# Optimization experiments

Hardware: AMD Instinct MI355X
Metric: run time of the kernel (lower is better)

Reference implementation:

```python
import jax, jax.numpy as jnp
import numpy as np
import itertools

DIM_X, DIM_Y = 3, 3
MAX_DIGIT = DIM_X * DIM_Y          # 9
NUM_NODES = MAX_DIGIT ** 2         # 81
EMBED = 16
HID = 96
BATCH = 256
ITERS = 4


def determine_edges(dim_x, dim_y):
    md = dim_x * dim_y
    rows = []
    for r in range(md):
        for c in range(md):
            s = {(r, i) for i in range(md)} | {(i, c) for i in range(md)}
            xm, ym = r // dim_x * dim_x, c // dim_y * dim_y
            s |= set(itertools.product(range(xm, xm + dim_x), range(ym, ym + dim_y)))
            s -= {(r, c)}
            rows.append(sorted(i * md + j for i, j in s))
    return np.asarray(rows, dtype=np.int32)  # [81, 20]


def mlp3(x, w0, b0, w1, b1, w2, b2):
    # MLP([a,b,c,d]): two ReLU hidden layers, linear output
    x = jax.nn.relu(x @ w0.T + b0)
    x = jax.nn.relu(x @ w1.T + b1)
    return x @ w2.T + b2


def setup_inputs() -> dict:
    key = jax.random.key(0)
    keys = iter(jax.random.split(key, 40))

    def lin(din, dout):
        kw, kb = jax.random.split(next(keys))
        lim = 1.0 / np.sqrt(din)
        w = jax.random.uniform(kw, (dout, din), jnp.float32, -lim, lim)
        b = jax.random.uniform(kb, (dout,), jnp.float32, -lim, lim)
        return w, b

    embed = jax.random.normal(next(keys), (MAX_DIGIT + 1, EMBED), jnp.float32)

    in_w0, in_b0 = lin(EMBED, HID); in_w1, in_b1 = lin(HID, HID); in_w2, in_b2 = lin(HID, HID)
    f_w0, f_b0 = lin(2 * HID, HID); f_w1, f_b1 = lin(HID, HID); f_w2, f_b2 = lin(HID, HID)
    g_w0, g_b0 = lin(2 * HID, HID); g_w1, g_b1 = lin(HID, HID); g_w2, g_b2 = lin(HID, HID)
    r_w0, r_b0 = lin(HID, HID); r_w1, r_b1 = lin(HID, HID); r_w2, r_b2 = lin(HID, MAX_DIGIT)

    lim = 1.0 / np.sqrt(HID)
    lstm_wih = jax.random.uniform(next(keys), (4 * HID, HID), jnp.float32, -lim, lim)
    lstm_whh = jax.random.uniform(next(keys), (4 * HID, HID), jnp.float32, -lim, lim)
    lstm_bih = jax.random.uniform(next(keys), (4 * HID,), jnp.float32, -lim, lim)
    lstm_bhh = jax.random.uniform(next(keys), (4 * HID,), jnp.float32, -lim, lim)

    grids = jax.random.randint(next(keys), (BATCH, NUM_NODES), 0, MAX_DIGIT + 1)
    c0 = jax.random.normal(next(keys), (BATCH * NUM_NODES, HID), jnp.float32)
    edges = jnp.asarray(determine_edges(DIM_X, DIM_Y))

    return dict(embed=embed,
                in_w0=in_w0, in_b0=in_b0, in_w1=in_w1, in_b1=in_b1, in_w2=in_w2, in_b2=in_b2,
                f_w0=f_w0, f_b0=f_b0, f_w1=f_w1, f_b1=f_b1, f_w2=f_w2, f_b2=f_b2,
                g_w0=g_w0, g_b0=g_b0, g_w1=g_w1, g_b1=g_b1, g_w2=g_w2, g_b2=g_b2,
                lstm_wih=lstm_wih, lstm_whh=lstm_whh, lstm_bih=lstm_bih, lstm_bhh=lstm_bhh,
                r_w0=r_w0, r_b0=r_b0, r_w1=r_w1, r_b1=r_b1, r_w2=r_w2, r_b2=r_b2,
                c0=c0, grids=grids, edges=edges, iters=ITERS)


def reference(embed,
              in_w0, in_b0, in_w1, in_b1, in_w2, in_b2,
              f_w0, f_b0, f_w1, f_b1, f_w2, f_b2,
              g_w0, g_b0, g_w1, g_b1, g_w2, g_b2,
              lstm_wih, lstm_whh, lstm_bih, lstm_bhh,
              r_w0, r_b0, r_w1, r_b1, r_w2, r_b2,
              c0, grids, edges, iters):
    B, N = grids.shape
    K = edges.shape[1]
    emb = embed[grids]                                   # [B, N, EMBED]
    X = mlp3(emb, in_w0, in_b0, in_w1, in_b1, in_w2, in_b2)  # [B, N, HID]
    H = X
    h = X.reshape(B * N, HID)
    c = c0
    outputs = []
    for _ in range(iters):
        # gather neighbor states: [B, N, K, HID]
        Hn = H[:, edges]
        Hs = jnp.broadcast_to(H[:, :, None, :], Hn.shape)
        pair = jnp.concatenate([Hs, Hn], axis=-1)        # [B, N, K, 2*HID]
        M = mlp3(pair, f_w0, f_b0, f_w1, f_b1, f_w2, f_b2).sum(axis=2)  # [B, N, HID]
        gin = mlp3(jnp.concatenate([X, M], axis=-1),
                   g_w0, g_b0, g_w1, g_b1, g_w2, g_b2).reshape(B * N, HID)
        # single-step LSTM (torch gate order: i, f, g, o)
        gates = gin @ lstm_wih.T + lstm_bih + h @ lstm_whh.T + lstm_bhh
        gi, gf, gg, go = jnp.split(gates, 4, axis=-1)
        c = jax.nn.sigmoid(gf) * c + jax.nn.sigmoid(gi) * jnp.tanh(gg)
        h = jax.nn.sigmoid(go) * jnp.tanh(c)
        H = h.reshape(B, N, HID)
        outputs.append(mlp3(H, r_w0, r_b0, r_w1, r_b1, r_w2, r_b2))  # [B, N, MAX_DIGIT]
    return jnp.stack(outputs)  # [iters, B, N, MAX_DIGIT]
```

## Files before the change

kernel.cpp:

```cpp
#include <hip/hip_runtime.h>
#include <hip/hip_bf16.h>

typedef __hip_bfloat16 bf16;
typedef __attribute__((ext_vector_type(8))) short short8;
typedef __attribute__((ext_vector_type(8))) __bf16 bf16x8;
typedef __attribute__((ext_vector_type(4))) float f32x4;

#define BN 20736
#define NNODE 81
#define KNB 20

__device__ inline float bf2f(short s) {
  union { unsigned u; float f; } x; x.u = ((unsigned)(unsigned short)s) << 16; return x.f;
}
__device__ inline short f2bf(float f) {
  __hip_bfloat16 h = __float2bfloat16(f);
  return *reinterpret_cast<short*>(&h);
}

__device__ inline void zacc3(f32x4 acc[3]) {
  #pragma unroll
  for (int nt = 0; nt < 3; ++nt) acc[nt] = (f32x4){0.f, 0.f, 0.f, 0.f};
}
__device__ inline void load_w48(const bf16* __restrict__ W, int ldw, int n0, int lr, int lq,
                                bf16x8 wf[3][3]) {
  #pragma unroll
  for (int nt = 0; nt < 3; ++nt)
    #pragma unroll
    for (int ks = 0; ks < 3; ++ks)
      wf[nt][ks] = __builtin_bit_cast(bf16x8,
          *(const short8*)&W[(size_t)(n0 + nt * 16 + lr) * ldw + ks * 32 + lq * 8]);
}
__device__ inline void gemm48(const bf16x8 af[3], const bf16x8 wf[3][3], f32x4 acc[3]) {
  #pragma unroll
  for (int ks = 0; ks < 3; ++ks)
    #pragma unroll
    for (int nt = 0; nt < 3; ++nt)
      acc[nt] = __builtin_amdgcn_mfma_f32_16x16x32_bf16(af[ks], wf[nt][ks], acc[nt], 0, 0, 0);
}
__device__ inline void acc_store_cs(float* xw, const f32x4 acc[3], int lr, int lq, int n0) {
  #pragma unroll
  for (int nt = 0; nt < 3; ++nt)
    #pragma unroll
    for (int r = 0; r < 4; ++r)
      xw[(lq * 4 + r) * 100 + n0 + nt * 16 + lr] = acc[nt][r];
}
__device__ inline void xbuf_frag(const float* xw, int lr, int lq,
                                 const float* __restrict__ bias, float bscale,
                                 const bf16* __restrict__ residRow, int act,
                                 bf16x8 af[3]) {
  #pragma unroll
  for (int ks = 0; ks < 3; ++ks) {
    const int c0 = ks * 32 + lq * 8;
    float4 x0 = *(const float4*)&xw[lr * 100 + c0];
    float4 x1 = *(const float4*)&xw[lr * 100 + c0 + 4];
    float xv[8] = {x0.x, x0.y, x0.z, x0.w, x1.x, x1.y, x1.z, x1.w};
    if (bias) {
      float4 b0 = *(const float4*)&bias[c0];
      float4 b1 = *(const float4*)&bias[c0 + 4];
      float bv[8] = {b0.x, b0.y, b0.z, b0.w, b1.x, b1.y, b1.z, b1.w};
      #pragma unroll
      for (int j = 0; j < 8; ++j) xv[j] += bscale * bv[j];
    }
    if (residRow) {
      short8 r8 = *(const short8*)&residRow[c0];
      #pragma unroll
      for (int j = 0; j < 8; ++j) xv[j] += bf2f(r8[j]);
    }
    short8 o;
    #pragma unroll
    for (int j = 0; j < 8; ++j) {
      float v = xv[j];
      if (act) v = fmaxf(v, 0.f);
      o[j] = f2bf(v);
    }
    af[ks] = __builtin_bit_cast(bf16x8, o);
  }
}
__device__ inline void store_frag(bf16* dst, int lq, const bf16x8 af[3]) {
  #pragma unroll
  for (int ks = 0; ks < 3; ++ks)
    *(short8*)&dst[ks * 32 + lq * 8] = __builtin_bit_cast(short8, af[ks]);
}

__global__ __launch_bounds__(256) void prep_k(
    const float* in_w1, const float* in_w2, const float* f_w1, const float* f_w2,
    const float* g_w1, const float* g_w2, const float* r_w0, const float* r_w1,
    const float* r_w2, const float* wih, const float* whh, const float* g_w0,
    const float* f_w0, const float* in_w0, const float* f_b0,
    bf16* inw1b, bf16* inw2b, bf16* fw1b, bf16* fw2b,
    bf16* gw1b, bf16* gw2b, bf16* rw0b, bf16* rw1b,
    bf16* rw2b, bf16* wihb, bf16* whhb, bf16* gw0b,
    bf16* wfnb, bf16* w0pb, float* bias_fn)
{
  int idx = blockIdx.x * 256 + threadIdx.x;
  int y = blockIdx.y;
  const float* src = nullptr; bf16* dst = nullptr; int cnt = 0;
  switch (y) {
    case 0:  src = in_w1; dst = inw1b; cnt = 9216;  break;
    case 1:  src = in_w2; dst = inw2b; cnt = 9216;  break;
    case 2:  src = f_w1;  dst = fw1b;  cnt = 9216;  break;
    case 3:  src = f_w2;  dst = fw2b;  cnt = 9216;  break;
    case 4:  src = g_w1;  dst = gw1b;  cnt = 9216;  break;
    case 5:  src = g_w2;  dst = gw2b;  cnt = 9216;  break;
    case 6:  src = r_w0;  dst = rw0b;  cnt = 9216;  break;
    case 7:  src = r_w1;  dst = rw1b;  cnt = 9216;  break;
    case 8:  src = r_w2;  dst = rw2b;  cnt = 864;   break;
    case 9:  src = wih;   dst = wihb;  cnt = 36864; break;
    case 10: src = whh;   dst = whhb;  cnt = 36864; break;
    case 11: src = g_w0;  dst = gw0b;  cnt = 18432; break;
    case 12: {
      if (idx < 18432) {
        int n = idx / 96, k = idx - n * 96;
        float v = (n < 96) ? f_w0[n * 192 + k] : f_w0[(n - 96) * 192 + 96 + k];
        wfnb[idx] = __float2bfloat16(v);
      }
      return;
    }
    case 13: {
      if (idx < 3072) {
        int n = idx >> 5, k = idx & 31;
        w0pb[idx] = __float2bfloat16(k < 16 ? in_w0[n * 16 + k] : 0.f);
      }
      return;
    }
    default: {
      if (idx < 192) bias_fn[idx] = (idx < 96) ? f_b0[idx] : 0.f;
      return;
    }
  }
  if (idx < cnt) dst[idx] = __float2bfloat16(src[idx]);
}

__global__ __launch_bounds__(256) void embed_k(const float* __restrict__ embed,
                                               const int* __restrict__ grids,
                                               bf16* __restrict__ emb) {
  int idx = blockIdx.x * 256 + threadIdx.x;
  if (idx >= BN * 32) return;
  int r = idx >> 5, k = idx & 31;
  emb[idx] = __float2bfloat16(k < 16 ? embed[grids[r] * 16 + k] : 0.f);
}

__global__ __launch_bounds__(256) void fused_in_k(
    const bf16* __restrict__ emb, const bf16* __restrict__ w0pb, const float* __restrict__ in_b0,
    const bf16* __restrict__ inw1b, const float* __restrict__ in_b1,
    const bf16* __restrict__ inw2b, const float* __restrict__ in_b2,
    const bf16* __restrict__ gw0b, const float* __restrict__ g_b0,
    const bf16* __restrict__ wfnb, const float* __restrict__ bias_fn,
    bf16* __restrict__ X, bf16* __restrict__ Xg, bf16* __restrict__ P)
{
  __shared__ float xbuf[2][2][1600];
  const int t = threadIdx.x, w = t >> 6, lane = t & 63, lr = lane & 15, lq = lane >> 4;
  const int mh = w >> 1, ch = w & 1, n0 = ch * 48;
  const int m0 = blockIdx.x * 32 + mh * 16;
  float* x0 = xbuf[0][mh];
  float* x1 = xbuf[1][mh];
  bf16x8 wf[3][3]; f32x4 acc[3]; bf16x8 af[3];

  bf16x8 a0 = __builtin_bit_cast(bf16x8, *(const short8*)&emb[(size_t)(m0 + lr) * 32 + lq * 8]);
  #pragma unroll
  for (int nt = 0; nt < 3; ++nt)
    wf[nt][0] = __builtin_bit_cast(bf16x8,
        *(const short8*)&w0pb[(size_t)(n0 + nt * 16 + lr) * 32 + lq * 8]);
  zacc3(acc);
  #pragma unroll
  for (int nt = 0; nt < 3; ++nt)
    acc[nt] = __builtin_amdgcn_mfma_f32_16x16x32_bf16(a0, wf[nt][0], acc[nt], 0, 0, 0);
  acc_store_cs(x0, acc, lr, lq, n0);
  __syncthreads();
  xbuf_frag(x0, lr, lq, in_b0, 1.f, nullptr, 1, af);
  load_w48(inw1b, 96, n0, lr, lq, wf); zacc3(acc); gemm48(af, wf, acc);
  acc_store_cs(x1, acc, lr, lq, n0);
  __syncthreads();
  xbuf_frag(x1, lr, lq, in_b1, 1.f, nullptr, 1, af);
  load_w48(inw2b, 96, n0, lr, lq, wf); zacc3(acc); gemm48(af, wf, acc);
  acc_store_cs(x0, acc, lr, lq, n0);
  __syncthreads();
  bf16x8 xf[3];
  xbuf_frag(x0, lr, lq, in_b2, 1.f, nullptr, 0, xf);
  if (ch == 0) store_frag(&X[(size_t)(m0 + lr) * 96], lq, xf);
  load_w48(gw0b, 192, n0, lr, lq, wf); zacc3(acc); gemm48(xf, wf, acc);
  acc_store_cs(x1, acc, lr, lq, n0);
  __syncthreads();
  xbuf_frag(x1, lr, lq, g_b0, 1.f, nullptr, 0, af);
  if (ch == 0) store_frag(&Xg[(size_t)(m0 + lr) * 96], lq, af);
  #pragma unroll
  for (int ph = 0; ph < 2; ++ph) {
    float* xb = ph ? x1 : x0;
    load_w48(wfnb + (size_t)ph * 96 * 96, 96, n0, lr, lq, wf); zacc3(acc); gemm48(xf, wf, acc);
    acc_store_cs(xb, acc, lr, lq, n0);
    __syncthreads();
    xbuf_frag(xb, lr, lq, bias_fn + ph * 96, 1.f, nullptr, 0, af);
    if (ch == 0) store_frag(&P[(size_t)(m0 + lr) * 192 + ph * 96], lq, af);
  }
}

__global__ __launch_bounds__(256) void edge_k(
    const bf16* __restrict__ P, const bf16* __restrict__ w1bf,
    const float* __restrict__ b1, const int* __restrict__ edges,
    const bf16* __restrict__ fw2b, const float* __restrict__ f_b2,
    bf16* __restrict__ M)
{
  __shared__ short zs[160 * 104];
  __shared__ short sbuf[16 * 104];
  const int t = threadIdx.x;
  const int ng0 = blockIdx.x * 2;
  for (int i = t; i < 8 * 104; i += 256) sbuf[(8 + i / 104) * 104 + (i % 104)] = 0;
  for (int cc = t; cc < 160 * 12; cc += 256) {
    int zrow = cc / 12, c8 = cc - zrow * 12;
    int g = zrow >= 80 ? 1 : 0;
    int row = zrow - g * 80;
    int p = row / 20, j = row - p * 20;
    int gr = (ng0 + g) * 4 + p;
    int b = gr / NNODE, i = gr - b * NNODE;
    int e = edges[i * KNB + j];
    short8 a8 = *(const short8*)&P[(size_t)gr * 192 + c8 * 8];
    short8 n8 = *(const short8*)&P[((size_t)b * NNODE + e) * 192 + 96 + c8 * 8];
    short8 z;
    #pragma unroll
    for (int q = 0; q < 8; ++q)
      z[q] = f2bf(fmaxf(bf2f(a8[q]) + bf2f(n8[q]), 0.f));
    *(short8*)&zs[zrow * 104 + c8 * 8] = z;
  }
  __syncthreads();

  const int w = t >> 6, lane = t & 63, lr = lane & 15, lq = lane >> 4;
  const int g = w >> 1, ch = w & 1, n0 = ch * 48, zb = g * 80;

  bf16x8 wf[3][3];
  #pragma unroll
  for (int nt = 0; nt < 3; ++nt)
    #pragma unroll
    for (int ks = 0; ks < 3; ++ks)
      wf[nt][ks] = __builtin_bit_cast(bf16x8,
          *(const short8*)&w1bf[(size_t)(n0 + nt * 16 + lr) * 96 + ks * 32 + lq * 8]);

  f32x4 acc[5][3];
  #pragma unroll
  for (int mt = 0; mt < 5; ++mt)
    #pragma unroll
    for (int nt = 0; nt < 3; ++nt) acc[mt][nt] = (f32x4){0.f, 0.f, 0.f, 0.f};

  #pragma unroll
  for (int ks = 0; ks < 3; ++ks) {
    const int koff = ks * 32 + lq * 8;
    #pragma unroll
    for (int mt = 0; mt < 5; ++mt) {
      bf16x8 af = __builtin_bit_cast(bf16x8, *(const short8*)&zs[(zb + mt * 16 + lr) * 104 + koff]);
      #pragma unroll
      for (int nt = 0; nt < 3; ++nt)
        acc[mt][nt] = __builtin_amdgcn_mfma_f32_16x16x32_bf16(af, wf[nt][ks], acc[mt][nt], 0, 0, 0);
    }
  }

  float bv[3];
  #pragma unroll
  for (int nt = 0; nt < 3; ++nt) bv[nt] = b1[n0 + nt * 16 + lr];
  float nodeacc[4][3];
  #pragma unroll
  for (int pp = 0; pp < 4; ++pp)
    #pragma unroll
    for (int nt = 0; nt < 3; ++nt) nodeacc[pp][nt] = 0.f;
  #pragma unroll
  for (int mt = 0; mt < 5; ++mt)
    #pragma unroll
    for (int nt = 0; nt < 3; ++nt)
      #pragma unroll
      for (int r = 0; r < 4; ++r) {
        int row = mt * 16 + lq * 4 + r;
        int p = row / 20;
        float v = fmaxf(acc[mt][nt][r] + bv[nt], 0.f);
        #pragma unroll
        for (int pp = 0; pp < 4; ++pp)
          nodeacc[pp][nt] += (p == pp) ? v : 0.f;
      }
  #pragma unroll
  for (int pp = 0; pp < 4; ++pp)
    #pragma unroll
    for (int nt = 0; nt < 3; ++nt) {
      float v = nodeacc[pp][nt];
      v += __shfl_xor(v, 16, 64);
      v += __shfl_xor(v, 32, 64);
      if (lq == 0)
        sbuf[(g * 4 + pp) * 104 + n0 + nt * 16 + lr] = f2bf(v);
    }
  __syncthreads();
  if (w < 2) {
    const int mn0 = w * 48;
    bf16x8 mwf[3][3];
    #pragma unroll
    for (int nt = 0; nt < 3; ++nt)
      #pragma unroll
      for (int ks = 0; ks < 3; ++ks)
        mwf[nt][ks] = __builtin_bit_cast(bf16x8,
            *(const short8*)&fw2b[(size_t)(mn0 + nt * 16 + lr) * 96 + ks * 32 + lq * 8]);
    f32x4 macc[3];
    zacc3(macc);
    #pragma unroll
    for (int ks = 0; ks < 3; ++ks) {
      bf16x8 af = __builtin_bit_cast(bf16x8, *(const short8*)&sbuf[lr * 104 + ks * 32 + lq * 8]);
      #pragma unroll
      for (int nt = 0; nt < 3; ++nt)
        macc[nt] = __builtin_amdgcn_mfma_f32_16x16x32_bf16(af, mwf[nt][ks], macc[nt], 0, 0, 0);
    }
    #pragma unroll
    for (int nt = 0; nt < 3; ++nt) {
      int col = mn0 + nt * 16 + lr;
      float bb = (float)KNB * f_b2[col];
      #pragma unroll
      for (int r = 0; r < 4; ++r) {
        int row = lq * 4 + r;
        if (row < 8)
          M[(size_t)(ng0 * 4 + row) * 96 + col] = __float2bfloat16(macc[nt][r] + bb);
      }
    }
  }
}

__global__ __launch_bounds__(256) void fused_mlp_k(
    const bf16* __restrict__ Min,
    const bf16* __restrict__ gw0b, const bf16* __restrict__ Xg,
    const bf16* __restrict__ gw1b, const float* __restrict__ g_b1,
    const bf16* __restrict__ gw2b, const float* __restrict__ g_b2,
    bf16* __restrict__ gin)
{
  __shared__ float xbuf[2][2][1600];
  const int t = threadIdx.x, w = t >> 6, lane = t & 63, lr = lane & 15, lq = lane >> 4;
  const int mh = w >> 1, ch = w & 1, n0 = ch * 48;
  const int m0 = blockIdx.x * 32 + mh * 16;
  float* x0 = xbuf[0][mh];
  float* x1 = xbuf[1][mh];
  bf16x8 wf[3][3]; f32x4 acc[3]; bf16x8 af[3];

  #pragma unroll
  for (int ks = 0; ks < 3; ++ks)
    af[ks] = __builtin_bit_cast(bf16x8,
        *(const short8*)&Min[(size_t)(m0 + lr) * 96 + ks * 32 + lq * 8]);
  load_w48(gw0b + 96, 192, n0, lr, lq, wf); zacc3(acc); gemm48(af, wf, acc);
  acc_store_cs(x0, acc, lr, lq, n0);
  __syncthreads();
  xbuf_frag(x0, lr, lq, nullptr, 0.f, &Xg[(size_t)(m0 + lr) * 96], 1, af);
  load_w48(gw1b, 96, n0, lr, lq, wf); zacc3(acc); gemm48(af, wf, acc);
  acc_store_cs(x1, acc, lr, lq, n0);
  __syncthreads();
  xbuf_frag(x1, lr, lq, g_b1, 1.f, nullptr, 1, af);
  load_w48(gw2b, 96, n0, lr, lq, wf); zacc3(acc); gemm48(af, wf, acc);
  acc_store_cs(x0, acc, lr, lq, n0);
  __syncthreads();
  xbuf_frag(x0, lr, lq, g_b2, 1.f, nullptr, 0, af);
  if (ch == 0) store_frag(&gin[(size_t)(m0 + lr) * 96], lq, af);
}

__global__ __launch_bounds__(256) void lstm_k(
    const bf16* __restrict__ gin, const bf16* __restrict__ Hin,
    const bf16* __restrict__ wihb, const bf16* __restrict__ whhb,
    const float* __restrict__ bih, const float* __restrict__ bhh,
    float* __restrict__ c, bf16* __restrict__ Hout)
{
  const int gslot = blockIdx.x * 4 + (threadIdx.x >> 6);
  const int rt = gslot / 6, knt = gslot - rt * 6;
  const int lane = threadIdx.x & 63, lr = lane & 15, lq = lane >> 4;
  const int m0 = rt * 16, kcol = knt * 16 + lr;

  f32x4 acc[4];
  #pragma unroll
  for (int g = 0; g < 4; ++g) acc[g] = (f32x4){0.f, 0.f, 0.f, 0.f};
  #pragma unroll
  for (int ks = 0; ks < 3; ++ks) {
    const int koff = ks * 32 + lq * 8;
    bf16x8 gf_ = __builtin_bit_cast(bf16x8, *(const short8*)&gin[(size_t)(m0 + lr) * 96 + koff]);
    bf16x8 hf_ = __builtin_bit_cast(bf16x8, *(const short8*)&Hin[(size_t)(m0 + lr) * 96 + koff]);
    #pragma unroll
    for (int g = 0; g < 4; ++g) {
      bf16x8 wi = __builtin_bit_cast(bf16x8, *(const short8*)&wihb[(size_t)(g * 96 + kcol) * 96 + koff]);
      acc[g] = __builtin_amdgcn_mfma_f32_16x16x32_bf16(gf_, wi, acc[g], 0, 0, 0);
      bf16x8 wh = __builtin_bit_cast(bf16x8, *(const short8*)&whhb[(size_t)(g * 96 + kcol) * 96 + koff]);
      acc[g] = __builtin_amdgcn_mfma_f32_16x16x32_bf16(hf_, wh, acc[g], 0, 0, 0);
    }
  }
  float bv[4];
  #pragma unroll
  for (int g = 0; g < 4; ++g) bv[g] = bih[g * 96 + kcol] + bhh[g * 96 + kcol];
  #pragma unroll
  for (int r = 0; r < 4; ++r) {
    int m = m0 + lq * 4 + r;
    size_t idx = (size_t)m * 96 + kcol;
    float gi = acc[0][r] + bv[0];
    float gf = acc[1][r] + bv[1];
    float gg = acc[2][r] + bv[2];
    float go = acc[3][r] + bv[3];
    float si = 1.f / (1.f + expf(-gi));
    float sf = 1.f / (1.f + expf(-gf));
    float so = 1.f / (1.f + expf(-go));
    float tg = tanhf(gg);
    float cn = sf * c[idx] + si * tg;
    c[idx] = cn;
    Hout[idx] = __float2bfloat16(so * tanhf(cn));
  }
}

__global__ __launch_bounds__(256) void fused_out_k(
    const bf16* __restrict__ H,
    const bf16* __restrict__ wfnb, const float* __restrict__ bias_fn, bf16* __restrict__ P,
    const bf16* __restrict__ rw0b, const float* __restrict__ r_b0,
    const bf16* __restrict__ rw1b, const float* __restrict__ r_b1,
    const bf16* __restrict__ rw2b, const float* __restrict__ r_b2,
    float* __restrict__ outp)
{
  __shared__ float xbuf[2][2][1600];
  const int t = threadIdx.x, w = t >> 6, lane = t & 63, lr = lane & 15, lq = lane >> 4;
  const int mh = w >> 1, ch = w & 1, n0 = ch * 48;
  const int m0 = blockIdx.x * 32 + mh * 16;
  float* x0 = xbuf[0][mh];
  float* x1 = xbuf[1][mh];
  bf16x8 wf[3][3]; f32x4 acc[3]; bf16x8 af[3];

  bf16x8 hf[3];
  #pragma unroll
  for (int ks = 0; ks < 3; ++ks)
    hf[ks] = __builtin_bit_cast(bf16x8,
        *(const short8*)&H[(size_t)(m0 + lr) * 96 + ks * 32 + lq * 8]);

  #pragma unroll
  for (int ph = 0; ph < 2; ++ph) {
    float* xb = ph ? x1 : x0;
    load_w48(wfnb + (size_t)ph * 96 * 96, 96, n0, lr, lq, wf); zacc3(acc); gemm48(hf, wf, acc);
    acc_store_cs(xb, acc, lr, lq, n0);
    __syncthreads();
    xbuf_frag(xb, lr, lq, bias_fn + ph * 96, 1.f, nullptr, 0, af);
    if (ch == 0) store_frag(&P[(size_t)(m0 + lr) * 192 + ph * 96], lq, af);
  }
  load_w48(rw0b, 96, n0, lr, lq, wf); zacc3(acc); gemm48(hf, wf, acc);
  acc_store_cs(x0, acc, lr, lq, n0);
  __syncthreads();
  xbuf_frag(x0, lr, lq, r_b0, 1.f, nullptr, 1, af);
  load_w48(rw1b, 96, n0, lr, lq, wf); zacc3(acc); gemm48(af, wf, acc);
  acc_store_cs(x1, acc, lr, lq, n0);
  __syncthreads();
  xbuf_frag(x1, lr, lq, r_b1, 1.f, nullptr, 1, af);
  if (ch == 0) {
    bf16x8 w9[3];
    #pragma unroll
    for (int ks = 0; ks < 3; ++ks) {
      short8 s = {0, 0, 0, 0, 0, 0, 0, 0};
      if (lr < 9) s = *(const short8*)&rw2b[(size_t)lr * 96 + ks * 32 + lq * 8];
      w9[ks] = __builtin_bit_cast(bf16x8, s);
    }
    f32x4 a9 = (f32x4){0.f, 0.f, 0.f, 0.f};
    #pragma unroll
    for (int ks = 0; ks < 3; ++ks)
      a9 = __builtin_amdgcn_mfma_f32_16x16x32_bf16(af[ks], w9[ks], a9, 0, 0, 0);
    if (lr < 9) {
      float bb = r_b2[lr];
      #pragma unroll
      for (int r = 0; r < 4; ++r)
        outp[(size_t)(m0 + lq * 4 + r) * 9 + lr] = a9[r] + bb;
    }
  }
}

extern "C" void kernel_launch(void* const* d_in, const int* in_sizes, int n_in,
                              void* d_out, int out_size, void* d_ws, size_t ws_size,
                              hipStream_t stream) {
  const float* embed   = (const float*)d_in[0];
  const float* in_w0   = (const float*)d_in[1];
  const float* in_b0   = (const float*)d_in[2];
  const float* in_w1   = (const float*)d_in[3];
  const float* in_b1   = (const float*)d_in[4];
  const float* in_w2   = (const float*)d_in[5];
  const float* in_b2   = (const float*)d_in[6];
  const float* f_w0    = (const float*)d_in[7];
  const float* f_b0    = (const float*)d_in[8];
  const float* f_w1    = (const float*)d_in[9];
  const float* f_b1    = (const float*)d_in[10];
  const float* f_w2    = (const float*)d_in[11];
  const float* f_b2    = (const float*)d_in[12];
  const float* g_w0    = (const float*)d_in[13];
  const float* g_b0    = (const float*)d_in[14];
  const float* g_w1    = (const float*)d_in[15];
  const float* g_b1    = (const float*)d_in[16];
  const float* g_w2    = (const float*)d_in[17];
  const float* g_b2    = (const float*)d_in[18];
  const float* wih     = (const float*)d_in[19];
  const float* whh     = (const float*)d_in[20];
  const float* bih     = (const float*)d_in[21];
  const float* bhh     = (const float*)d_in[22];
  const float* r_w0    = (const float*)d_in[23];
  const float* r_b0    = (const float*)d_in[24];
  const float* r_w1    = (const float*)d_in[25];
  const float* r_b1    = (const float*)d_in[26];
  const float* r_w2    = (const float*)d_in[27];
  const float* r_b2    = (const float*)d_in[28];
  const float* c0      = (const float*)d_in[29];
  const int*   grids   = (const int*)d_in[30];
  const int*   edges   = (const int*)d_in[31];

  float* out = (float*)d_out;
  const int iters = out_size / (BN * 9);

  float* c    = (float*)d_ws;
  bf16* H0    = (bf16*)(c + (size_t)BN * 96);
  bf16* H1    = H0 + (size_t)BN * 96;
  bf16* Xg    = H1 + (size_t)BN * 96;
  bf16* P     = Xg + (size_t)BN * 96;
  bf16* Mb    = P  + (size_t)BN * 192;
  bf16* gin   = Mb + (size_t)BN * 96;
  bf16* emb   = gin + (size_t)BN * 96;
  bf16* w0pb  = emb + (size_t)BN * 32;
  bf16* wfnb  = w0pb + 3072;
  bf16* inw1b = wfnb + 18432;
  bf16* inw2b = inw1b + 9216;
  bf16* fw1b  = inw2b + 9216;
  bf16* fw2b  = fw1b + 9216;
  bf16* gw0b  = fw2b + 9216;
  bf16* gw1b  = gw0b + 18432;
  bf16* gw2b  = gw1b + 9216;
  bf16* rw0b  = gw2b + 9216;
  bf16* rw1b  = rw0b + 9216;
  bf16* rw2b  = rw1b + 9216;
  bf16* wihb  = rw2b + 864;
  bf16* whhb  = wihb + 36864;
  float* bias_fn = (float*)(whhb + 36864);

  prep_k<<<dim3(144, 15), 256, 0, stream>>>(
      in_w1, in_w2, f_w1, f_w2, g_w1, g_w2, r_w0, r_w1, r_w2, wih, whh, g_w0,
      f_w0, in_w0, f_b0,
      inw1b, inw2b, fw1b, fw2b, gw1b, gw2b, rw0b, rw1b, rw2b, wihb, whhb, gw0b,
      wfnb, w0pb, bias_fn);
  embed_k<<<(BN * 32) / 256, 256, 0, stream>>>(embed, grids, emb);
  fused_in_k<<<BN / 32, 256, 0, stream>>>(emb, w0pb, in_b0, inw1b, in_b1, inw2b, in_b2,
                                          gw0b, g_b0, wfnb, bias_fn, H0, Xg, P);
  hipMemcpyAsync(c, c0, (size_t)BN * 96 * sizeof(float), hipMemcpyDeviceToDevice, stream);

  for (int it = 0; it < iters; ++it) {
    bf16* Hin  = (it & 1) ? H1 : H0;
    bf16* Hout = (it & 1) ? H0 : H1;
    edge_k<<<BN / 8, 256, 0, stream>>>(P, fw1b, f_b1, edges, fw2b, f_b2, Mb);
    fused_mlp_k<<<BN / 32, 256, 0, stream>>>(Mb, gw0b, Xg, gw1b, g_b1, gw2b, g_b2, gin);
    lstm_k<<<BN * 6 / 64, 256, 0, stream>>>(gin, Hin, wihb, whhb, bih, bhh, c, Hout);
    fused_out_k<<<BN / 32, 256, 0, stream>>>(Hout, wfnb, bias_fn, P, rw0b, r_b0,
                                             rw1b, r_b1, rw2b, r_b2,
                                             out + (size_t)it * BN * 9);
  }
}
```

Before: 361.4 us.

## Fuse g-MLP, LSTM cell and output/projection kernels into one per-iteration kernel

Merges the g-MLP, LSTM and output kernels into a single kernel per iteration. The gin and H intermediates now stay in registers and shared memory instead of round-tripping through global memory, which also saves two launches per iteration. The P projection is skipped on the last iteration, where nothing reads it. In exchange, each wave holds 12 LSTM gate accumulators and loads larger weight slices, which raises register pressure and may lower occupancy.

```diff
diff --git a/kernel.cpp b/kernel.cpp
--- a/kernel.cpp
+++ b/kernel.cpp
@@ -17,6 +17,9 @@
   __hip_bfloat16 h = __float2bfloat16(f);
   return *reinterpret_cast<short*>(&h);
 }
+__device__ inline bf16x8 ld8(const bf16* p) {
+  return __builtin_bit_cast(bf16x8, *(const short8*)p);
+}
 
 __device__ inline void zacc3(f32x4 acc[3]) {
   #pragma unroll
@@ -28,8 +31,7 @@
   for (int nt = 0; nt < 3; ++nt)
     #pragma unroll
     for (int ks = 0; ks < 3; ++ks)
-      wf[nt][ks] = __builtin_bit_cast(bf16x8,
-          *(const short8*)&W[(size_t)(n0 + nt * 16 + lr) * ldw + ks * 32 + lq * 8]);
+      wf[nt][ks] = ld8(&W[(size_t)(n0 + nt * 16 + lr) * ldw + ks * 32 + lq * 8]);
 }
 __device__ inline void gemm48(const bf16x8 af[3], const bf16x8 wf[3][3], f32x4 acc[3]) {
   #pragma unroll
@@ -157,11 +159,10 @@
   float* x1 = xbuf[1][mh];
   bf16x8 wf[3][3]; f32x4 acc[3]; bf16x8 af[3];
 
-  bf16x8 a0 = __builtin_bit_cast(bf16x8, *(const short8*)&emb[(size_t)(m0 + lr) * 32 + lq * 8]);
+  bf16x8 a0 = ld8(&emb[(size_t)(m0 + lr) * 32 + lq * 8]);
   #pragma unroll
   for (int nt = 0; nt < 3; ++nt)
-    wf[nt][0] = __builtin_bit_cast(bf16x8,
-        *(const short8*)&w0pb[(size_t)(n0 + nt * 16 + lr) * 32 + lq * 8]);
+    wf[nt][0] = ld8(&w0pb[(size_t)(n0 + nt * 16 + lr) * 32 + lq * 8]);
   zacc3(acc);
   #pragma unroll
   for (int nt = 0; nt < 3; ++nt)
@@ -232,8 +233,7 @@
   for (int nt = 0; nt < 3; ++nt)
     #pragma unroll
     for (int ks = 0; ks < 3; ++ks)
-      wf[nt][ks] = __builtin_bit_cast(bf16x8,
-          *(const short8*)&w1bf[(size_t)(n0 + nt * 16 + lr) * 96 + ks * 32 + lq * 8]);
+      wf[nt][ks] = ld8(&w1bf[(size_t)(n0 + nt * 16 + lr) * 96 + ks * 32 + lq * 8]);
 
   f32x4 acc[5][3];
   #pragma unroll
@@ -292,8 +292,7 @@
     for (int nt = 0; nt < 3; ++nt)
       #pragma unroll
       for (int ks = 0; ks < 3; ++ks)
-        mwf[nt][ks] = __builtin_bit_cast(bf16x8,
-            *(const short8*)&fw2b[(size_t)(mn0 + nt * 16 + lr) * 96 + ks * 32 + lq * 8]);
+        mwf[nt][ks] = ld8(&fw2b[(size_t)(mn0 + nt * 16 + lr) * 96 + ks * 32 + lq * 8]);
     f32x4 macc[3];
     zacc3(macc);
     #pragma unroll
@@ -317,12 +316,20 @@
   }
 }
 
-__global__ __launch_bounds__(256) void fused_mlp_k(
+__global__ __launch_bounds__(256) void fused_iter_k(
     const bf16* __restrict__ Min,
     const bf16* __restrict__ gw0b, const bf16* __restrict__ Xg,
     const bf16* __restrict__ gw1b, const float* __restrict__ g_b1,
     const bf16* __restrict__ gw2b, const float* __restrict__ g_b2,
-    bf16* __restrict__ gin)
+    const bf16* __restrict__ Hin,
+    const bf16* __restrict__ wihb, const bf16* __restrict__ whhb,
+    const float* __restrict__ bih, const float* __restrict__ bhh,
+    float* __restrict__ c, bf16* __restrict__ Hout,
+    const bf16* __restrict__ wfnb, const float* __restrict__ bias_fn, bf16* __restrict__ P,
+    const bf16* __restrict__ rw0b, const float* __restrict__ r_b0,
+    const bf16* __restrict__ rw1b, const float* __restrict__ r_b1,
+    const bf16* __restrict__ rw2b, const float* __restrict__ r_b2,
+    float* __restrict__ outp, int doP)
 {
   __shared__ float xbuf[2][2][1600];
   const int t = threadIdx.x, w = t >> 6, lane = t & 63, lr = lane & 15, lq = lane >> 4;
@@ -334,8 +341,7 @@
 
   #pragma unroll
   for (int ks = 0; ks < 3; ++ks)
-    af[ks] = __builtin_bit_cast(bf16x8,
-        *(const short8*)&Min[(size_t)(m0 + lr) * 96 + ks * 32 + lq * 8]);
+    af[ks] = ld8(&Min[(size_t)(m0 + lr) * 96 + ks * 32 + lq * 8]);
   load_w48(gw0b + 96, 192, n0, lr, lq, wf); zacc3(acc); gemm48(af, wf, acc);
   acc_store_cs(x0, acc, lr, lq, n0);
   __syncthreads();
@@ -347,89 +353,73 @@
   load_w48(gw2b, 96, n0, lr, lq, wf); zacc3(acc); gemm48(af, wf, acc);
   acc_store_cs(x0, acc, lr, lq, n0);
   __syncthreads();
-  xbuf_frag(x0, lr, lq, g_b2, 1.f, nullptr, 0, af);
-  if (ch == 0) store_frag(&gin[(size_t)(m0 + lr) * 96], lq, af);
-}
-
-__global__ __launch_bounds__(256) void lstm_k(
-    const bf16* __restrict__ gin, const bf16* __restrict__ Hin,
-    const bf16* __restrict__ wihb, const bf16* __restrict__ whhb,
-    const float* __restrict__ bih, const float* __restrict__ bhh,
-    float* __restrict__ c, bf16* __restrict__ Hout)
-{
-  const int gslot = blockIdx.x * 4 + (threadIdx.x >> 6);
-  const int rt = gslot / 6, knt = gslot - rt * 6;
-  const int lane = threadIdx.x & 63, lr = lane & 15, lq = lane >> 4;
-  const int m0 = rt * 16, kcol = knt * 16 + lr;
-
-  f32x4 acc[4];
-  #pragma unroll
-  for (int g = 0; g < 4; ++g) acc[g] = (f32x4){0.f, 0.f, 0.f, 0.f};
-  #pragma unroll
-  for (int ks = 0; ks < 3; ++ks) {
-    const int koff = ks * 32 + lq * 8;
-    bf16x8 gf_ = __builtin_bit_cast(bf16x8, *(const short8*)&gin[(size_t)(m0 + lr) * 96 + koff]);
-    bf16x8 hf_ = __builtin_bit_cast(bf16x8, *(const short8*)&Hin[(size_t)(m0 + lr) * 96 + koff]);
-    #pragma unroll
-    for (int g = 0; g < 4; ++g) {
-      bf16x8 wi = __builtin_bit_cast(bf16x8, *(const short8*)&wihb[(size_t)(g * 96 + kcol) * 96 + koff]);
-      acc[g] = __builtin_amdgcn_mfma_f32_16x16x32_bf16(gf_, wi, acc[g], 0, 0, 0);
-      bf16x8 wh = __builtin_bit_cast(bf16x8, *(const short8*)&whhb[(size_t)(g * 96 + kcol) * 96 + koff]);
-      acc[g] = __builtin_amdgcn_mfma_f32_16x16x32_bf16(hf_, wh, acc[g], 0, 0, 0);
-    }
-  }
-  float bv[4];
-  #pragma unroll
-  for (int g = 0; g < 4; ++g) bv[g] = bih[g * 96 + kcol] + bhh[g * 96 + kcol];
-  #pragma unroll
-  for (int r = 0; r < 4; ++r) {
-    int m = m0 + lq * 4 + r;
-    size_t idx = (size_t)m * 96 + kcol;
-    float gi = acc[0][r] + bv[0];
-    float gf = acc[1][r] + bv[1];
-    float gg = acc[2][r] + bv[2];
-    float go = acc[3][r] + bv[3];
-    float si = 1.f / (1.f + expf(-gi));
-    float sf = 1.f / (1.f + expf(-gf));
-    float so = 1.f / (1.f + expf(-go));
-    float tg = tanhf(gg);
-    float cn = sf * c[idx] + si * tg;
-    c[idx] = cn;
-    Hout[idx] = __float2bfloat16(so * tanhf(cn));
-  }
-}
-
-__global__ __launch_bounds__(256) void fused_out_k(
-    const bf16* __restrict__ H,
-    const bf16* __restrict__ wfnb, const float* __restrict__ bias_fn, bf16* __restrict__ P,
-    const bf16* __restrict__ rw0b, const float* __restrict__ r_b0,
-    const bf16* __restrict__ rw1b, const float* __restrict__ r_b1,
-    const bf16* __restrict__ rw2b, const float* __restrict__ r_b2,
-    float* __restrict__ outp)
-{
-  __shared__ float xbuf[2][2][1600];
-  const int t = threadIdx.x, w = t >> 6, lane = t & 63, lr = lane & 15, lq = lane >> 4;
-  const int mh = w >> 1, ch = w & 1, n0 = ch * 48;
-  const int m0 = blockIdx.x * 32 + mh * 16;
-  float* x0 = xbuf[0][mh];
-  float* x1 = xbuf[1][mh];
-  bf16x8 wf[3][3]; f32x4 acc[3]; bf16x8 af[3];
-
+  bf16x8 gf[3];
+  xbuf_frag(x0, lr, lq, g_b2, 1.f, nullptr, 0, gf);
+
+  bf16x8 hin[3];
+  #pragma unroll
+  for (int ks = 0; ks < 3; ++ks)
+    hin[ks] = ld8(&Hin[(size_t)(m0 + lr) * 96 + ks * 32 + lq * 8]);
+  f32x4 ga[4][3];
+  #pragma unroll
+  for (int g4 = 0; g4 < 4; ++g4)
+    #pragma unroll
+    for (int nt = 0; nt < 3; ++nt) ga[g4][nt] = (f32x4){0.f, 0.f, 0.f, 0.f};
+  #pragma unroll
+  for (int g4 = 0; g4 < 4; ++g4)
+    #pragma unroll
+    for (int nt = 0; nt < 3; ++nt) {
+      size_t nrow = (size_t)(g4 * 96 + n0 + nt * 16 + lr) * 96;
+      #pragma unroll
+      for (int ks = 0; ks < 3; ++ks) {
+        ga[g4][nt] = __builtin_amdgcn_mfma_f32_16x16x32_bf16(
+            gf[ks], ld8(&wihb[nrow + ks * 32 + lq * 8]), ga[g4][nt], 0, 0, 0);
+        ga[g4][nt] = __builtin_amdgcn_mfma_f32_16x16x32_bf16(
+            hin[ks], ld8(&whhb[nrow + ks * 32 + lq * 8]), ga[g4][nt], 0, 0, 0);
+      }
+    }
+  #pragma unroll
+  for (int nt = 0; nt < 3; ++nt) {
+    int col = n0 + nt * 16 + lr;
+    float bvi = bih[col] + bhh[col];
+    float bvf = bih[96 + col] + bhh[96 + col];
+    float bvg = bih[192 + col] + bhh[192 + col];
+    float bvo = bih[288 + col] + bhh[288 + col];
+    #pragma unroll
+    for (int r = 0; r < 4; ++r) {
+      int m = m0 + lq * 4 + r;
+      size_t idx = (size_t)m * 96 + col;
+      float gi = ga[0][nt][r] + bvi;
+      float gfv = ga[1][nt][r] + bvf;
+      float gg = ga[2][nt][r] + bvg;
+      float go = ga[3][nt][r] + bvo;
+      float si = 1.f / (1.f + expf(-gi));
+      float sf = 1.f / (1.f + expf(-gfv));
+      float so = 1.f / (1.f + expf(-go));
+      float tg = tanhf(gg);
+      float cn = sf * c[idx] + si * tg;
+      c[idx] = cn;
+      float ho = so * tanhf(cn);
+      Hout[idx] = __float2bfloat16(ho);
+      x1[(lq * 4 + r) * 100 + col] = ho;
+    }
+  }
+  __syncthreads();
   bf16x8 hf[3];
-  #pragma unroll
-  for (int ks = 0; ks < 3; ++ks)
-    hf[ks] = __builtin_bit_cast(bf16x8,
-        *(const short8*)&H[(size_t)(m0 + lr) * 96 + ks * 32 + lq * 8]);
-
-  #pragma unroll
-  for (int ph = 0; ph < 2; ++ph) {
-    float* xb = ph ? x1 : x0;
-    load_w48(wfnb + (size_t)ph * 96 * 96, 96, n0, lr, lq, wf); zacc3(acc); gemm48(hf, wf, acc);
-    acc_store_cs(xb, acc, lr, lq, n0);
-    __syncthreads();
-    xbuf_frag(xb, lr, lq, bias_fn + ph * 96, 1.f, nullptr, 0, af);
-    if (ch == 0) store_frag(&P[(size_t)(m0 + lr) * 192 + ph * 96], lq, af);
-  }
+  xbuf_frag(x1, lr, lq, nullptr, 0.f, nullptr, 0, hf);
+
+  if (doP) {
+    #pragma unroll
+    for (int ph = 0; ph < 2; ++ph) {
+      float* xb = ph ? x1 : x0;
+      load_w48(wfnb + (size_t)ph * 96 * 96, 96, n0, lr, lq, wf); zacc3(acc); gemm48(hf, wf, acc);
+      acc_store_cs(xb, acc, lr, lq, n0);
+      __syncthreads();
+      xbuf_frag(xb, lr, lq, bias_fn + ph * 96, 1.f, nullptr, 0, af);
+      if (ch == 0) store_frag(&P[(size_t)(m0 + lr) * 192 + ph * 96], lq, af);
+    }
+  }
+
   load_w48(rw0b, 96, n0, lr, lq, wf); zacc3(acc); gemm48(hf, wf, acc);
   acc_store_cs(x0, acc, lr, lq, n0);
   __syncthreads();
@@ -504,8 +494,7 @@
   bf16* Xg    = H1 + (size_t)BN * 96;
   bf16* P     = Xg + (size_t)BN * 96;
   bf16* Mb    = P  + (size_t)BN * 192;
-  bf16* gin   = Mb + (size_t)BN * 96;
-  bf16* emb   = gin + (size_t)BN * 96;
+  bf16* emb   = Mb + (size_t)BN * 96;
   bf16* w0pb  = emb + (size_t)BN * 32;
   bf16* wfnb  = w0pb + 3072;
   bf16* inw1b = wfnb + 18432;
@@ -536,10 +525,10 @@
     bf16* Hin  = (it & 1) ? H1 : H0;
     bf16* Hout = (it & 1) ? H0 : H1;
     edge_k<<<BN / 8, 256, 0, stream>>>(P, fw1b, f_b1, edges, fw2b, f_b2, Mb);
-    fused_mlp_k<<<BN / 32, 256, 0, stream>>>(Mb, gw0b, Xg, gw1b, g_b1, gw2b, g_b2, gin);
-    lstm_k<<<BN * 6 / 64, 256, 0, stream>>>(gin, Hin, wihb, whhb, bih, bhh, c, Hout);
-    fused_out_k<<<BN / 32, 256, 0, stream>>>(Hout, wfnb, bias_fn, P, rw0b, r_b0,
-                                             rw1b, r_b1, rw2b, r_b2,
-                                             out + (size_t)it * BN * 9);
-  }
-}
+    fused_iter_k<<<BN / 32, 256, 0, stream>>>(
+        Mb, gw0b, Xg, gw1b, g_b1, gw2b, g_b2,
+        Hin, wihb, whhb, bih, bhh, c, Hout,
+        wfnb, bias_fn, P, rw0b, r_b0, rw1b, r_b1, rw2b, r_b2,
+        out + (size_t)it * BN * 9, it < iters - 1 ? 1 : 0);
+  }
+}
```

Measured after the change: 336.5 us. 6.9% less time.
